# Performance work log

Hardware: AMD Instinct MI355X
Metric: run time of the kernel (lower is better)

The kernel has to match this reference:

```python
import jax, jax.numpy as jnp
import numpy as np

N_FEAT = 16
N_MF = 7
N_CLASSES = 10
N_RULES = 512
BATCH = 16384


def setup_inputs() -> dict:
    key = jax.random.key(0)
    k1, k2, k3, k4 = jax.random.split(key, 4)
    x = jax.random.normal(k1, (N_FEAT, BATCH), dtype=jnp.float32)
    # Triangular MF params (a < b < c): centers spread over data range, fixed width,
    # plus small per-feature jitter to break symmetry.
    centers = jnp.linspace(-2.0, 2.0, N_MF, dtype=jnp.float32)  # [M]
    jitter = 0.05 * jax.random.normal(k2, (N_FEAT, N_MF), dtype=jnp.float32)
    b = centers[None, :] + jitter                                # [F, M]
    width = jnp.float32(1.0)
    mf_abc = jnp.stack([b - width, b, b + width], axis=-1)       # [F, M, 3]
    rule_conditions = jax.random.randint(k3, (N_RULES, N_FEAT), 0, N_MF, dtype=jnp.int32)
    rule_classes = jax.random.randint(k4, (N_RULES,), 0, N_CLASSES, dtype=jnp.int32)
    return {"x": x, "mf_abc": mf_abc, "rule_conditions": rule_conditions,
            "rule_classes": rule_classes}


def _memberships(x, mf_abc):
    # x: [F, B]; mf_abc: [F, M, 3] -> memberships [F, M, B]
    a = mf_abc[..., 0][..., None]  # [F, M, 1]
    b = mf_abc[..., 1][..., None]
    c = mf_abc[..., 2][..., None]
    xe = x[:, None, :]             # [F, 1, B]
    left = (xe - a) / (b - a)
    right = (c - xe) / (c - b)
    return jnp.clip(jnp.minimum(left, right), 0.0, 1.0)


def reference(x, mf_abc, rule_conditions, rule_classes):
    mem = _memberships(x, mf_abc)                       # [F, M, B]
    feat_idx = jnp.arange(N_FEAT)[None, :]              # [1, F]
    gathered = mem[feat_idx, rule_conditions, :]        # [R, F, B]  (per-rule gather)
    firing = gathered.min(axis=1)                       # [R, B]     (RuleDef.eval min)
    class_sum = jax.ops.segment_sum(firing, rule_classes,
                                    num_segments=N_CLASSES)  # [C, B]
    return class_sum.T                                  # [B, C] (stack dim=1)
```

## Files before the change

### kernel.cpp

```cpp
#include <hip/hip_runtime.h>
#include <hip/hip_bf16.h>

#define NFEAT    16
#define NMF      7
#define NCLASSES 10
#define NRULES   512
#define BATCH    16384

#define WAVES 8
#define BLOCK (WAVES * 64)

static_assert(BATCH % 64 == 0, "");
static_assert(NRULES == BLOCK, "one rule per thread in stage 2");

__global__ __launch_bounds__(BLOCK) void nefclass_kernel(
    const float* __restrict__ x,
    const float* __restrict__ mf_abc,
    const int*   __restrict__ rcond,
    const int*   __restrict__ rcls,
    float*       __restrict__ out)
{
    __shared__ unsigned long long lmask[NFEAT * NMF];
    __shared__ float mem[NFEAT * NMF][64];
    __shared__ float acc[WAVES][NCLASSES][64];

    const int tid   = threadIdx.x;
    const int lane  = tid & 63;
    const int wave  = tid >> 6;
    const int sbase = blockIdx.x * 64;

    const int r0 = wave * 64;
    const int r  = r0 + lane;
    const int4* rc = (const int4*)(rcond + r * NFEAT);
    const int4 c0 = rc[0], c1 = rc[1], c2 = rc[2], c3 = rc[3];

    const int   f0  = wave * 2;
    const float xv0 = x[(f0 + 0) * BATCH + sbase + lane];
    const float xv1 = x[(f0 + 1) * BATCH + sbase + lane];
    #pragma unroll
    for (int ff = 0; ff < 2; ++ff) {
        const float xv = ff ? xv1 : xv0;
        const int   f  = f0 + ff;
        #pragma unroll
        for (int m = 0; m < NMF; ++m) {
            const int p = f * NMF + m;
            const float a = mf_abc[p * 3 + 0];
            const float c = mf_abc[p * 3 + 2];
            const unsigned long long bm = __ballot(xv > a && xv < c);
            if (lane == 0) lmask[p] = bm;
        }
    }
    __syncthreads();

    unsigned long long rm = lmask[ 0 * NMF + c0.x];
    rm &= lmask[ 1 * NMF + c0.y];
    rm &= lmask[ 2 * NMF + c0.z];
    rm &= lmask[ 3 * NMF + c0.w];
    rm &= lmask[ 4 * NMF + c1.x];
    rm &= lmask[ 5 * NMF + c1.y];
    rm &= lmask[ 6 * NMF + c1.z];
    rm &= lmask[ 7 * NMF + c1.w];
    rm &= lmask[ 8 * NMF + c2.x];
    rm &= lmask[ 9 * NMF + c2.y];
    rm &= lmask[10 * NMF + c2.z];
    rm &= lmask[11 * NMF + c2.w];
    rm &= lmask[12 * NMF + c3.x];
    rm &= lmask[13 * NMF + c3.y];
    rm &= lmask[14 * NMF + c3.z];
    rm &= lmask[15 * NMF + c3.w];

    unsigned long long fired = __ballot(rm != 0ull);
    const int any = __syncthreads_or(fired != 0ull ? 1 : 0);

    if (!any) {
        if (tid < 64 * NCLASSES / 4)
            ((float4*)(out + sbase * NCLASSES))[tid] = make_float4(0.f, 0.f, 0.f, 0.f);
        return;
    }

    #pragma unroll
    for (int ff = 0; ff < 2; ++ff) {
        const float xv = ff ? xv1 : xv0;
        const int   f  = f0 + ff;
        #pragma unroll
        for (int m = 0; m < NMF; ++m) {
            const int p = f * NMF + m;
            const float a = mf_abc[p * 3 + 0];
            const float b = mf_abc[p * 3 + 1];
            const float c = mf_abc[p * 3 + 2];
            float v = fminf((xv - a) / (b - a), (c - xv) / (c - b));
            mem[p][lane] = fminf(fmaxf(v, 0.0f), 1.0f);
        }
    }
    #pragma unroll
    for (int c = 0; c < NCLASSES; ++c) acc[wave][c][lane] = 0.0f;
    __syncthreads();

    while (fired != 0ull) {
        const int b = __ffsll(fired) - 1;
        fired &= fired - 1;
        const int rr = r0 + b;
        float fir = 1.0f;
        #pragma unroll
        for (int f = 0; f < NFEAT; ++f) {
            const int m = rcond[rr * NFEAT + f];
            fir = fminf(fir, mem[f * NMF + m][lane]);
        }
        const int c = rcls[rr];
        acc[wave][c][lane] += fir;
    }
    __syncthreads();

    for (int o = tid; o < 64 * NCLASSES; o += BLOCK) {
        const int s = o / NCLASSES;
        const int c = o - s * NCLASSES;
        float vsum = 0.0f;
        #pragma unroll
        for (int w = 0; w < WAVES; ++w) vsum += acc[w][c][s];
        out[sbase * NCLASSES + o] = vsum;
    }
}

extern "C" void kernel_launch(void* const* d_in, const int* in_sizes, int n_in,
                              void* d_out, int out_size, void* d_ws, size_t ws_size,
                              hipStream_t stream)
{
    const float* x     = (const float*)d_in[0];
    const float* mf    = (const float*)d_in[1];
    const int*   rcond = (const int*)d_in[2];
    const int*   rcls  = (const int*)d_in[3];
    float*       out   = (float*)d_out;

    nefclass_kernel<<<dim3(BATCH / 64), dim3(BLOCK), 0, stream>>>(x, mf, rcond, rcls, out);
}
```

Before: 11.31 us.

## Use single-wave blocks that handle all rules per wave sequentially

Each block shrinks from 8 waves to one 64-lane wave. That wave loads all 16 features, builds every membership ballot mask, and checks all 512 rules in 8 passes. This removes cross-wave synchronization, the per-wave accumulator reduction and the block-wide OR barrier. The cost is a longer serial chain per wave, since 8x more rule-mask work and gather loads run per block, and 256 blocks of only 64 threads give low occupancy on the GPU.

```diff
diff --git a/kernel.cpp b/kernel.cpp
--- a/kernel.cpp
+++ b/kernel.cpp
@@ -7,13 +7,9 @@
 #define NRULES   512
 #define BATCH    16384
 
-#define WAVES 8
-#define BLOCK (WAVES * 64)
+static_assert(BATCH % 64 == 0, "");
 
-static_assert(BATCH % 64 == 0, "");
-static_assert(NRULES == BLOCK, "one rule per thread in stage 2");
-
-__global__ __launch_bounds__(BLOCK) void nefclass_kernel(
+__global__ __launch_bounds__(64) void nefclass_kernel(
     const float* __restrict__ x,
     const float* __restrict__ mf_abc,
     const int*   __restrict__ rcond,
@@ -22,102 +18,104 @@
 {
     __shared__ unsigned long long lmask[NFEAT * NMF];
     __shared__ float mem[NFEAT * NMF][64];
-    __shared__ float acc[WAVES][NCLASSES][64];
+    __shared__ float acc[NCLASSES][64];
 
-    const int tid   = threadIdx.x;
-    const int lane  = tid & 63;
-    const int wave  = tid >> 6;
+    const int lane  = threadIdx.x;
     const int sbase = blockIdx.x * 64;
 
-    const int r0 = wave * 64;
-    const int r  = r0 + lane;
-    const int4* rc = (const int4*)(rcond + r * NFEAT);
-    const int4 c0 = rc[0], c1 = rc[1], c2 = rc[2], c3 = rc[3];
+    float xv[NFEAT];
+    #pragma unroll
+    for (int f = 0; f < NFEAT; ++f) xv[f] = x[f * BATCH + sbase + lane];
 
-    const int   f0  = wave * 2;
-    const float xv0 = x[(f0 + 0) * BATCH + sbase + lane];
-    const float xv1 = x[(f0 + 1) * BATCH + sbase + lane];
     #pragma unroll
-    for (int ff = 0; ff < 2; ++ff) {
-        const float xv = ff ? xv1 : xv0;
-        const int   f  = f0 + ff;
+    for (int f = 0; f < NFEAT; ++f) {
         #pragma unroll
         for (int m = 0; m < NMF; ++m) {
             const int p = f * NMF + m;
             const float a = mf_abc[p * 3 + 0];
             const float c = mf_abc[p * 3 + 2];
-            const unsigned long long bm = __ballot(xv > a && xv < c);
+            const unsigned long long bm = __ballot(xv[f] > a && xv[f] < c);
             if (lane == 0) lmask[p] = bm;
         }
     }
     __syncthreads();
 
-    unsigned long long rm = lmask[ 0 * NMF + c0.x];
-    rm &= lmask[ 1 * NMF + c0.y];
-    rm &= lmask[ 2 * NMF + c0.z];
-    rm &= lmask[ 3 * NMF + c0.w];
-    rm &= lmask[ 4 * NMF + c1.x];
-    rm &= lmask[ 5 * NMF + c1.y];
-    rm &= lmask[ 6 * NMF + c1.z];
-    rm &= lmask[ 7 * NMF + c1.w];
-    rm &= lmask[ 8 * NMF + c2.x];
-    rm &= lmask[ 9 * NMF + c2.y];
-    rm &= lmask[10 * NMF + c2.z];
-    rm &= lmask[11 * NMF + c2.w];
-    rm &= lmask[12 * NMF + c3.x];
-    rm &= lmask[13 * NMF + c3.y];
-    rm &= lmask[14 * NMF + c3.z];
-    rm &= lmask[15 * NMF + c3.w];
+    unsigned long long firedm[8];
+    unsigned long long anyf = 0ull;
+    #pragma unroll
+    for (int pass = 0; pass < 8; ++pass) {
+        const int r = pass * 64 + lane;
+        const int4* rc = (const int4*)(rcond + r * NFEAT);
+        const int4 c0 = rc[0], c1 = rc[1], c2 = rc[2], c3 = rc[3];
+        unsigned long long rm = lmask[ 0 * NMF + c0.x];
+        rm &= lmask[ 1 * NMF + c0.y];
+        rm &= lmask[ 2 * NMF + c0.z];
+        rm &= lmask[ 3 * NMF + c0.w];
+        rm &= lmask[ 4 * NMF + c1.x];
+        rm &= lmask[ 5 * NMF + c1.y];
+        rm &= lmask[ 6 * NMF + c1.z];
+        rm &= lmask[ 7 * NMF + c1.w];
+        rm &= lmask[ 8 * NMF + c2.x];
+        rm &= lmask[ 9 * NMF + c2.y];
+        rm &= lmask[10 * NMF + c2.z];
+        rm &= lmask[11 * NMF + c2.w];
+        rm &= lmask[12 * NMF + c3.x];
+        rm &= lmask[13 * NMF + c3.y];
+        rm &= lmask[14 * NMF + c3.z];
+        rm &= lmask[15 * NMF + c3.w];
+        firedm[pass] = __ballot(rm != 0ull);
+        anyf |= firedm[pass];
+    }
 
-    unsigned long long fired = __ballot(rm != 0ull);
-    const int any = __syncthreads_or(fired != 0ull ? 1 : 0);
-
-    if (!any) {
-        if (tid < 64 * NCLASSES / 4)
-            ((float4*)(out + sbase * NCLASSES))[tid] = make_float4(0.f, 0.f, 0.f, 0.f);
+    if (anyf == 0ull) {
+        const float4 z = make_float4(0.f, 0.f, 0.f, 0.f);
+        float4* o4 = (float4*)(out + sbase * NCLASSES);
+        o4[lane]      = z;
+        o4[64 + lane] = z;
+        if (lane < 32) o4[128 + lane] = z;
         return;
     }
 
     #pragma unroll
-    for (int ff = 0; ff < 2; ++ff) {
-        const float xv = ff ? xv1 : xv0;
-        const int   f  = f0 + ff;
+    for (int f = 0; f < NFEAT; ++f) {
         #pragma unroll
         for (int m = 0; m < NMF; ++m) {
             const int p = f * NMF + m;
             const float a = mf_abc[p * 3 + 0];
             const float b = mf_abc[p * 3 + 1];
             const float c = mf_abc[p * 3 + 2];
-            float v = fminf((xv - a) / (b - a), (c - xv) / (c - b));
+            float v = fminf((xv[f] - a) / (b - a), (c - xv[f]) / (c - b));
             mem[p][lane] = fminf(fmaxf(v, 0.0f), 1.0f);
         }
     }
     #pragma unroll
-    for (int c = 0; c < NCLASSES; ++c) acc[wave][c][lane] = 0.0f;
+    for (int c = 0; c < NCLASSES; ++c) acc[c][lane] = 0.0f;
     __syncthreads();
 
-    while (fired != 0ull) {
-        const int b = __ffsll(fired) - 1;
-        fired &= fired - 1;
-        const int rr = r0 + b;
-        float fir = 1.0f;
-        #pragma unroll
-        for (int f = 0; f < NFEAT; ++f) {
-            const int m = rcond[rr * NFEAT + f];
-            fir = fminf(fir, mem[f * NMF + m][lane]);
+    #pragma unroll
+    for (int pass = 0; pass < 8; ++pass) {
+        unsigned long long fm = firedm[pass];
+        while (fm) {
+            const int b = __ffsll(fm) - 1;
+            fm &= fm - 1;
+            const int rr = pass * 64 + b;
+            float fir = 1.0f;
+            #pragma unroll
+            for (int f = 0; f < NFEAT; ++f) {
+                const int m = rcond[rr * NFEAT + f];
+                fir = fminf(fir, mem[f * NMF + m][lane]);
+            }
+            acc[rcls[rr]][lane] += fir;
         }
-        const int c = rcls[rr];
-        acc[wave][c][lane] += fir;
     }
     __syncthreads();
 
-    for (int o = tid; o < 64 * NCLASSES; o += BLOCK) {
+    #pragma unroll
+    for (int i = 0; i < NCLASSES; ++i) {
+        const int o = i * 64 + lane;
         const int s = o / NCLASSES;
         const int c = o - s * NCLASSES;
-        float vsum = 0.0f;
-        #pragma unroll
-        for (int w = 0; w < WAVES; ++w) vsum += acc[w][c][s];
-        out[sbase * NCLASSES + o] = vsum;
+        out[sbase * NCLASSES + o] = acc[c][s];
     }
 }
 
@@ -131,5 +129,5 @@
     const int*   rcls  = (const int*)d_in[3];
     float*       out   = (float*)d_out;
 
-    nefclass_kernel<<<dim3(BATCH / 64), dim3(BLOCK), 0, stream>>>(x, mf, rcond, rcls, out);
+    nefclass_kernel<<<dim3(BATCH / 64), dim3(64), 0, stream>>>(x, mf, rcond, rcls, out);
 }
```

Measured after the change: 25.85 us. +128.6%, slower.
